# Kernel tuning notes

Measured on AMD Instinct MI355X. Metric: run time of the kernel, lower is better.

Reference implementation:

```python
import jax, jax.numpy as jnp
import numpy as np

T, IN, OUT = 16384, 4096, 4096


def setup_inputs() -> dict:
    key = jax.random.key(0)
    k1, k2, k3, k4, k5 = jax.random.split(key, 5)
    x = jax.random.randint(k1, (T, IN), -128, 128, dtype=jnp.int32)      # int8-valued activations
    weight = jax.random.randint(k2, (OUT, IN), -128, 128, dtype=jnp.int32)  # int8-valued weights
    bias = jax.random.randint(k3, (OUT,), -128, 128, dtype=jnp.int32)    # int8-valued bias
    # requant scales: alpha = a_scale*w_scale/o_scale, beta = b_scale/o_scale
    alpha = jax.random.uniform(k4, (1,), jnp.float32, 1e-4, 1e-3)
    beta = jax.random.uniform(k5, (1,), jnp.float32, 0.5, 1.5)
    return {"x": x, "weight": weight, "bias": bias, "alpha": alpha, "beta": beta}


def reference(x, weight, bias, alpha, beta):
    # INT8 GEMM with int32 accumulation: acc[t,o] = sum_i x[t,i] * W[o,i]
    acc = jnp.einsum('ti,oi->to', x, weight,
                     preferred_element_type=jnp.int32)  # [T, OUT] int32
    # inline dequant + bias + requant epilogue
    y = acc.astype(jnp.float32) * alpha + bias.astype(jnp.float32) * beta
    # round and saturate to int8 output (W8A8B8O8)
    out = jnp.clip(jnp.round(y), -128.0, 127.0).astype(jnp.int8)
    return out
```

## Files before the change

### kernel.cpp

```cpp
#include <hip/hip_runtime.h>
#include <stdint.h>

constexpr int T_DIM   = 16384;
constexpr int IN_DIM  = 4096;
constexpr int OUT_DIM = 4096;

using int32x4  = __attribute__((ext_vector_type(4)))  int;
using int32x16 = __attribute__((ext_vector_type(16))) int;

#define GLOAD_LDS16(g, l)                                                     \
    __builtin_amdgcn_global_load_lds(                                         \
        (const __attribute__((address_space(1))) void*)(uintptr_t)(g),        \
        (__attribute__((address_space(3))) void*)(uintptr_t)(l), 16, 0, 0)

__global__ void pack_swz(const int* __restrict__ src, int8_t* __restrict__ dst,
                         int rows, int cols) {
    int64_t tid = (int64_t)blockIdx.x * blockDim.x + threadIdx.x;
    int64_t nchunks = (int64_t)rows * (cols / 16);
    if (tid >= nchunks) return;
    int row  = (int)(tid / (cols / 16));
    int cidx = (int)(tid % (cols / 16));
    const int32x4* s4 =
        reinterpret_cast<const int32x4*>(src + (int64_t)row * cols + (cidx << 4));
    uint32_t p[4];
#pragma unroll
    for (int v = 0; v < 4; ++v) {
        int32x4 t = s4[v];
        p[v] = (uint32_t)(t[0] & 0xff) | ((uint32_t)(t[1] & 0xff) << 8) |
               ((uint32_t)(t[2] & 0xff) << 16) | ((uint32_t)(t[3] & 0xff) << 24);
    }
    int cs = (cidx & ~7) | ((cidx & 7) ^ (row & 7));
    *reinterpret_cast<int32x4*>(dst + (int64_t)row * cols + (cs << 4)) =
        *reinterpret_cast<int32x4*>(p);
}

constexpr int BM = 256, BN = 256, BK = 128;
constexpr int NT    = IN_DIM / BK;
constexpr int ATILE = BM * BK;
constexpr int BUFSZ = 2 * ATILE;

__global__ __launch_bounds__(512, 2)
void gemm_i8_32(const int8_t* __restrict__ x8, const int8_t* __restrict__ w8,
                const int* __restrict__ bias, const float* __restrict__ alphap,
                const float* __restrict__ betap, int* __restrict__ out) {
    __shared__ __align__(16) int8_t lds[2 * BUFSZ];

    const int tid  = threadIdx.x;
    const int lane = tid & 63;
    const int wid  = tid >> 6;
    const int wr   = wid >> 2;
    const int wc   = wid & 3;

    const int nwg = gridDim.x;
    const int cpx = nwg >> 3;
    const int bid = blockIdx.x;
    const int swz = (bid & 7) * cpx + (bid >> 3);
    const int bm  = swz >> 4;
    const int bn  = swz & 15;
    const int brow = bm * BM;
    const int bcol = bn * BN;

    const float alpha = *alphap;
    const float beta  = *betap;

    const int lrow  = lane & 31;
    const int khalf = lane >> 5;

    const int8_t* pA[4];
    const int8_t* pB[4];
    int dA[4], dB[4];
#pragma unroll
    for (int l = 0; l < 4; ++l) {
        const int off = l * 8192 + tid * 16;
        const int row = off >> 7, in = off & 127;
        pA[l] = x8 + (int64_t)(brow + row) * IN_DIM + in;
        pB[l] = w8 + (int64_t)(bcol + row) * IN_DIM + in;
        dA[l] = off;
        dB[l] = ATILE + off;
    }

    int aoff[4], boff[2];
#pragma unroll
    for (int m = 0; m < 4; ++m) {
        const int row = wr * 128 + m * 32 + lrow;
        aoff[m] = row * BK + ((khalf ^ (row & 7)) << 4);
    }
#pragma unroll
    for (int n = 0; n < 2; ++n) {
        const int row = wc * 64 + n * 32 + lrow;
        boff[n] = ATILE + row * BK + ((khalf ^ (row & 7)) << 4);
    }

    int32x16 acc[4][2] = {};

#define STAGE8(DSTB)                                                          \
    do {                                                                      \
        int8_t* nb = lds + (DSTB) * BUFSZ;                                    \
        _Pragma("unroll") for (int l = 0; l < 4; ++l) {                       \
            GLOAD_LDS16(pA[l], nb + dA[l]);                                   \
            GLOAD_LDS16(pB[l], nb + dB[l]);                                   \
            pA[l] += BK; pB[l] += BK;                                         \
        }                                                                     \
    } while (0)

#define TILE(RB, SB, PF, LAST)                                                \
    do {                                                                      \
        const int8_t* rb = lds + (RB) * BUFSZ;                                \
        if (PF) STAGE8(SB);                                                   \
        _Pragma("unroll") for (int ks = 0; ks < 4; ++ks) {                    \
            int32x4 bf0 = *reinterpret_cast<const int32x4*>(                  \
                rb + (boff[0] ^ (ks << 5)));                                  \
            int32x4 bf1 = *reinterpret_cast<const int32x4*>(                  \
                rb + (boff[1] ^ (ks << 5)));                                  \
            int32x4 af[4];                                                    \
            _Pragma("unroll") for (int m = 0; m < 4; ++m)                     \
                af[m] = *reinterpret_cast<const int32x4*>(                    \
                    rb + (aoff[m] ^ (ks << 5)));                              \
            __builtin_amdgcn_s_setprio(1);                                    \
            _Pragma("unroll") for (int m = 0; m < 4; ++m) {                   \
                acc[m][0] = __builtin_amdgcn_mfma_i32_32x32x32_i8(            \
                    af[m], bf0, acc[m][0], 0, 0, 0);                          \
                acc[m][1] = __builtin_amdgcn_mfma_i32_32x32x32_i8(            \
                    af[m], bf1, acc[m][1], 0, 0, 0);                          \
            }                                                                 \
            __builtin_amdgcn_s_setprio(0);                                    \
        }                                                                     \
        if (!(LAST)) {                                                        \
            asm volatile("s_waitcnt vmcnt(0)" ::: "memory");                  \
            __builtin_amdgcn_s_barrier();                                     \
            asm volatile("" ::: "memory");                                    \
        }                                                                     \
    } while (0)

    STAGE8(0);
    asm volatile("s_waitcnt vmcnt(0)" ::: "memory");
    __builtin_amdgcn_s_barrier();
    asm volatile("" ::: "memory");

#pragma unroll 1
    for (int tt = 0; tt < NT - 2; tt += 2) {
        TILE(0, 1, true, false);
        TILE(1, 0, true, false);
    }
    TILE(0, 1, true,  false);
    TILE(1, 0, false, true);
#undef TILE
#undef STAGE8

#pragma unroll
    for (int n = 0; n < 2; ++n) {
        const int col = bcol + wc * 64 + n * 32 + lrow;
        const float bterm = (float)bias[col] * beta;
#pragma unroll
        for (int m = 0; m < 4; ++m) {
            const int rbase = brow + wr * 128 + m * 32 + khalf * 4;
#pragma unroll
            for (int q = 0; q < 4; ++q) {
#pragma unroll
                for (int j = 0; j < 4; ++j) {
                    float y = (float)acc[m][n][q * 4 + j] * alpha + bterm;
                    y = rintf(y);
                    y = fminf(fmaxf(y, -128.0f), 127.0f);
                    out[(int64_t)(rbase + q * 8 + j) * OUT_DIM + col] = (int)y;
                }
            }
        }
    }
}

__global__ __launch_bounds__(256)
void gemm_i8_fb(const int* __restrict__ x32, const int* __restrict__ w32,
                const int* __restrict__ bias, const float* __restrict__ alphap,
                const float* __restrict__ betap, int* __restrict__ out) {
    constexpr int FBM = 128, FBK = 128;
    __shared__ int8_t lA[FBM * FBK];
    __shared__ int8_t lB[FBM * FBK];

    const int tid  = threadIdx.x;
    const int wid  = tid >> 6;
    const int lane = tid & 63;
    const int nwg = gridDim.x;
    const int cpx = nwg >> 3;
    const int bid = blockIdx.x;
    const int swz = (bid & 7) * cpx + (bid >> 3);
    const int brow = (swz >> 5) * FBM;
    const int bcol = (swz & 31) * FBM;
    const int wr = wid >> 1, wc = wid & 1;
    const float alpha = *alphap;
    const float beta  = *betap;

    int32x4 acc[4][4] = {};
    for (int kt = 0; kt < IN_DIM / FBK; ++kt) {
        const int64_t kbase = (int64_t)kt * FBK;
#pragma unroll
        for (int q = 0; q < 4; ++q) {
            const int off = wid * 4096 + q * 1024 + lane * 16;
            const int row = off >> 7;
            const int k   = off & 127;
            const int* ga = x32 + (int64_t)(brow + row) * IN_DIM + kbase + k;
            const int* gb = w32 + (int64_t)(bcol + row) * IN_DIM + kbase + k;
            uint32_t pa[4], pb[4];
#pragma unroll
            for (int v = 0; v < 4; ++v) {
                int32x4 ta = reinterpret_cast<const int32x4*>(ga)[v];
                int32x4 tb = reinterpret_cast<const int32x4*>(gb)[v];
                pa[v] = (uint32_t)(ta[0] & 0xff) | ((uint32_t)(ta[1] & 0xff) << 8) |
                        ((uint32_t)(ta[2] & 0xff) << 16) | ((uint32_t)(ta[3] & 0xff) << 24);
                pb[v] = (uint32_t)(tb[0] & 0xff) | ((uint32_t)(tb[1] & 0xff) << 8) |
                        ((uint32_t)(tb[2] & 0xff) << 16) | ((uint32_t)(tb[3] & 0xff) << 24);
            }
            const int sc = ((k >> 4) ^ (row & 7)) << 4;
            *reinterpret_cast<int32x4*>(lA + row * FBK + sc) = *reinterpret_cast<int32x4*>(pa);
            *reinterpret_cast<int32x4*>(lB + row * FBK + sc) = *reinterpret_cast<int32x4*>(pb);
        }
        __syncthreads();
#pragma unroll
        for (int ks = 0; ks < 2; ++ks) {
            const int gg = lane >> 4, rr = lane & 15;
            const int lc = ks * 4 + gg;
            int32x4 af[4], bf[4];
#pragma unroll
            for (int m = 0; m < 4; ++m) {
                const int row = wr * 64 + m * 16 + rr;
                af[m] = *reinterpret_cast<const int32x4*>(lA + row * FBK + ((lc ^ (row & 7)) << 4));
            }
#pragma unroll
            for (int n = 0; n < 4; ++n) {
                const int row = wc * 64 + n * 16 + rr;
                bf[n] = *reinterpret_cast<const int32x4*>(lB + row * FBK + ((lc ^ (row & 7)) << 4));
            }
#pragma unroll
            for (int m = 0; m < 4; ++m)
#pragma unroll
                for (int n = 0; n < 4; ++n)
                    acc[m][n] = __builtin_amdgcn_mfma_i32_16x16x64_i8(af[m], bf[n], acc[m][n], 0, 0, 0);
        }
        __syncthreads();
    }
    const int r4 = (lane >> 4) * 4;
    const int cl = lane & 15;
#pragma unroll
    for (int n = 0; n < 4; ++n) {
        const int col = bcol + wc * 64 + n * 16 + cl;
        const float bterm = (float)bias[col] * beta;
#pragma unroll
        for (int m = 0; m < 4; ++m) {
            const int row0 = brow + wr * 64 + m * 16 + r4;
#pragma unroll
            for (int j = 0; j < 4; ++j) {
                float y = (float)acc[m][n][j] * alpha + bterm;
                y = rintf(y);
                y = fminf(fmaxf(y, -128.0f), 127.0f);
                out[(int64_t)(row0 + j) * OUT_DIM + col] = (int)y;
            }
        }
    }
}

extern "C" void kernel_launch(void* const* d_in, const int* in_sizes, int n_in,
                              void* d_out, int out_size, void* d_ws, size_t ws_size,
                              hipStream_t stream) {
    const int*   x     = (const int*)d_in[0];
    const int*   w     = (const int*)d_in[1];
    const int*   bias  = (const int*)d_in[2];
    const float* alpha = (const float*)d_in[3];
    const float* beta  = (const float*)d_in[4];
    int*         out   = (int*)d_out;

    const size_t need = (size_t)T_DIM * IN_DIM + (size_t)OUT_DIM * IN_DIM;

    if (ws_size >= need) {
        int8_t* x8 = (int8_t*)d_ws;
        int8_t* w8 = x8 + (size_t)T_DIM * IN_DIM;
        {
            int64_t nch = (int64_t)T_DIM * (IN_DIM / 16);
            pack_swz<<<(int)((nch + 255) / 256), 256, 0, stream>>>(x, x8, T_DIM, IN_DIM);
        }
        {
            int64_t nch = (int64_t)OUT_DIM * (IN_DIM / 16);
            pack_swz<<<(int)((nch + 255) / 256), 256, 0, stream>>>(w, w8, OUT_DIM, IN_DIM);
        }
        const int grid = (T_DIM / BM) * (OUT_DIM / BN);
        gemm_i8_32<<<grid, 512, 0, stream>>>(x8, w8, bias, alpha, beta, out);
    } else {
        const int grid = (T_DIM / 128) * (OUT_DIM / 128);
        gemm_i8_fb<<<grid, 256, 0, stream>>>(x, w, bias, alpha, beta, out);
    }
}
```

Baseline: 388.8 us.

## Pack int8 operands into MFMA fragment-major blocks for conflict-free LDS reads

The pack kernel now stores the int8 operands as 32x32 fragment blocks: each 1 KB block holds two 512-byte halves with 16 bytes per row, so the layout matches what each MFMA lane reads. The GEMM stages whole contiguous 1 KB blocks per wave into LDS and reads fragments at lane*16 offsets, with no XOR swizzle and simpler address math. Global loads become fully contiguous per wave and LDS reads should be free of bank conflicts. In exchange, the pack kernel's writes are scattered, and correctness now depends on the block indexing matching the MFMA operand layout.

After: 417.3 us. 7.3% more time.

```diff
diff --git a/kernel.cpp b/kernel.cpp
--- a/kernel.cpp
+++ b/kernel.cpp
@@ -13,15 +13,15 @@
         (const __attribute__((address_space(1))) void*)(uintptr_t)(g),        \
         (__attribute__((address_space(3))) void*)(uintptr_t)(l), 16, 0, 0)
 
-__global__ void pack_swz(const int* __restrict__ src, int8_t* __restrict__ dst,
-                         int rows, int cols) {
+__global__ void pack_fm(const int* __restrict__ src, int8_t* __restrict__ dst,
+                        int rows, int cols) {
     int64_t tid = (int64_t)blockIdx.x * blockDim.x + threadIdx.x;
     int64_t nchunks = (int64_t)rows * (cols / 16);
     if (tid >= nchunks) return;
-    int row  = (int)(tid / (cols / 16));
-    int cidx = (int)(tid % (cols / 16));
+    int row = (int)(tid / (cols / 16));
+    int kc  = (int)(tid % (cols / 16));
     const int32x4* s4 =
-        reinterpret_cast<const int32x4*>(src + (int64_t)row * cols + (cidx << 4));
+        reinterpret_cast<const int32x4*>(src + (int64_t)row * cols + (kc << 4));
     uint32_t p[4];
 #pragma unroll
     for (int v = 0; v < 4; ++v) {
@@ -29,9 +29,9 @@
         p[v] = (uint32_t)(t[0] & 0xff) | ((uint32_t)(t[1] & 0xff) << 8) |
                ((uint32_t)(t[2] & 0xff) << 16) | ((uint32_t)(t[3] & 0xff) << 24);
     }
-    int cs = (cidx & ~7) | ((cidx & 7) ^ (row & 7));
-    *reinterpret_cast<int32x4*>(dst + (int64_t)row * cols + (cs << 4)) =
-        *reinterpret_cast<int32x4*>(p);
+    const int64_t blk = (int64_t)(row >> 5) * (cols >> 5) + (kc >> 1);
+    const int64_t off = blk * 1024 + (kc & 1) * 512 + (row & 31) * 16;
+    *reinterpret_cast<int32x4*>(dst + off) = *reinterpret_cast<int32x4*>(p);
 }
 
 constexpr int BM = 256, BN = 256, BK = 128;
@@ -40,7 +40,7 @@
 constexpr int BUFSZ = 2 * ATILE;
 
 __global__ __launch_bounds__(512, 2)
-void gemm_i8_32(const int8_t* __restrict__ x8, const int8_t* __restrict__ w8,
+void gemm_i8_fm(const int8_t* __restrict__ x8p, const int8_t* __restrict__ w8p,
                 const int* __restrict__ bias, const float* __restrict__ alphap,
                 const float* __restrict__ betap, int* __restrict__ out) {
     __shared__ __align__(16) int8_t lds[2 * BUFSZ];
@@ -66,40 +66,32 @@
     const int lrow  = lane & 31;
     const int khalf = lane >> 5;
 
+    constexpr int KT_ROW = IN_DIM >> 5;
     const int8_t* pA[4];
     const int8_t* pB[4];
     int dA[4], dB[4];
 #pragma unroll
-    for (int l = 0; l < 4; ++l) {
-        const int off = l * 8192 + tid * 16;
-        const int row = off >> 7, in = off & 127;
-        pA[l] = x8 + (int64_t)(brow + row) * IN_DIM + in;
-        pB[l] = w8 + (int64_t)(bcol + row) * IN_DIM + in;
-        dA[l] = off;
-        dB[l] = ATILE + off;
-    }
-
-    int aoff[4], boff[2];
-#pragma unroll
-    for (int m = 0; m < 4; ++m) {
-        const int row = wr * 128 + m * 32 + lrow;
-        aoff[m] = row * BK + ((khalf ^ (row & 7)) << 4);
-    }
-#pragma unroll
-    for (int n = 0; n < 2; ++n) {
-        const int row = wc * 64 + n * 32 + lrow;
-        boff[n] = ATILE + row * BK + ((khalf ^ (row & 7)) << 4);
-    }
+    for (int j = 0; j < 4; ++j) {
+        const int b  = j * 8 + wid;
+        const int rt = b >> 2, kt = b & 3;
+        pA[j] = x8p + ((int64_t)((brow >> 5) + rt) * KT_ROW + kt) * 1024 + lane * 16;
+        pB[j] = w8p + ((int64_t)((bcol >> 5) + rt) * KT_ROW + kt) * 1024 + lane * 16;
+        dA[j] = b * 1024 + lane * 16;
+        dB[j] = ATILE + b * 1024 + lane * 16;
+    }
+
+    const int abase = (wr << 14) + lane * 16;
+    const int bbase = ATILE + (wc << 13) + lane * 16;
 
     int32x16 acc[4][2] = {};
 
 #define STAGE8(DSTB)                                                          \
     do {                                                                      \
         int8_t* nb = lds + (DSTB) * BUFSZ;                                    \
-        _Pragma("unroll") for (int l = 0; l < 4; ++l) {                       \
-            GLOAD_LDS16(pA[l], nb + dA[l]);                                   \
-            GLOAD_LDS16(pB[l], nb + dB[l]);                                   \
-            pA[l] += BK; pB[l] += BK;                                         \
+        _Pragma("unroll") for (int j = 0; j < 4; ++j) {                       \
+            GLOAD_LDS16(pA[j], nb + dA[j]);                                   \
+            GLOAD_LDS16(pB[j], nb + dB[j]);                                   \
+            pA[j] += 4096; pB[j] += 4096;                                     \
         }                                                                     \
     } while (0)
 
@@ -109,13 +101,13 @@
         if (PF) STAGE8(SB);                                                   \
         _Pragma("unroll") for (int ks = 0; ks < 4; ++ks) {                    \
             int32x4 bf0 = *reinterpret_cast<const int32x4*>(                  \
-                rb + (boff[0] ^ (ks << 5)));                                  \
+                rb + bbase + (0 * 4 + ks) * 1024);                            \
             int32x4 bf1 = *reinterpret_cast<const int32x4*>(                  \
-                rb + (boff[1] ^ (ks << 5)));                                  \
+                rb + bbase + (1 * 4 + ks) * 1024);                            \
             int32x4 af[4];                                                    \
             _Pragma("unroll") for (int m = 0; m < 4; ++m)                     \
                 af[m] = *reinterpret_cast<const int32x4*>(                    \
-                    rb + (aoff[m] ^ (ks << 5)));                              \
+                    rb + abase + (m * 4 + ks) * 1024);                        \
             __builtin_amdgcn_s_setprio(1);                                    \
             _Pragma("unroll") for (int m = 0; m < 4; ++m) {                   \
                 acc[m][0] = __builtin_amdgcn_mfma_i32_32x32x32_i8(            \
@@ -270,18 +262,18 @@
     const size_t need = (size_t)T_DIM * IN_DIM + (size_t)OUT_DIM * IN_DIM;
 
     if (ws_size >= need) {
-        int8_t* x8 = (int8_t*)d_ws;
-        int8_t* w8 = x8 + (size_t)T_DIM * IN_DIM;
+        int8_t* x8p = (int8_t*)d_ws;
+        int8_t* w8p = x8p + (size_t)T_DIM * IN_DIM;
         {
             int64_t nch = (int64_t)T_DIM * (IN_DIM / 16);
-            pack_swz<<<(int)((nch + 255) / 256), 256, 0, stream>>>(x, x8, T_DIM, IN_DIM);
+            pack_fm<<<(int)((nch + 255) / 256), 256, 0, stream>>>(x, x8p, T_DIM, IN_DIM);
         }
         {
             int64_t nch = (int64_t)OUT_DIM * (IN_DIM / 16);
-            pack_swz<<<(int)((nch + 255) / 256), 256, 0, stream>>>(w, w8, OUT_DIM, IN_DIM);
+            pack_fm<<<(int)((nch + 255) / 256), 256, 0, stream>>>(w, w8p, OUT_DIM, IN_DIM);
         }
         const int grid = (T_DIM / BM) * (OUT_DIM / BN);
-        gemm_i8_32<<<grid, 512, 0, stream>>>(x8, w8, bias, alpha, beta, out);
+        gemm_i8_fm<<<grid, 512, 0, stream>>>(x8p, w8p, bias, alpha, beta, out);
     } else {
         const int grid = (T_DIM / 128) * (OUT_DIM / 128);
         gemm_i8_fb<<<grid, 256, 0, stream>>>(x, w, bias, alpha, beta, out);
```
